# Performance work log

Hardware: AMD Instinct MI355X
Metric: run time of the kernel (lower is better)

Reference implementation:

```python
import jax, jax.numpy as jnp
import numpy as np

NEG_SLOPE = 0.2


def _gat_layer(x, src, dst, W, a_src, a_dst, b, concat):
    """PyG-style GATConv (with self-loops already appended to src/dst).
    x: [N, Fin], W: [Fin, H*D], a_src/a_dst: [H, D], b: [H*D] or [D].
    """
    N = x.shape[0]
    H, D = a_src.shape
    h = (x @ W).reshape(N, H, D)                      # per-head projections
    es = jnp.einsum('nhd,hd->nh', h, a_src)           # alpha_src per node
    ed = jnp.einsum('nhd,hd->nh', h, a_dst)           # alpha_dst per node
    e = jax.nn.leaky_relu(es[src] + ed[dst], NEG_SLOPE)   # [E, H] edge logits
    # segment softmax over incoming edges of each target node
    m = jax.ops.segment_max(e, dst, num_segments=N)       # [N, H]
    ex = jnp.exp(e - m[dst])
    s = jax.ops.segment_sum(ex, dst, num_segments=N)      # [N, H]
    alpha = ex / jnp.where(s > 0, s, 1.0)[dst]            # [E, H]
    out = jax.ops.segment_sum(h[src] * alpha[:, :, None], dst, num_segments=N)  # [N,H,D]
    out = out.reshape(N, H * D) if concat else out.mean(axis=1)
    return out + b


def setup_inputs() -> dict:
    key = jax.random.key(0)
    ks = jax.random.split(key, 16)
    N, E, F_IN, HID, HEADS, NG, NC = 50000, 1000000, 128, 64, 4, 512, 2
    x = jax.random.normal(ks[0], (N, F_IN), dtype=jnp.float32)
    edge_index = jax.random.randint(ks[1], (2, E), 0, N, dtype=jnp.int32)
    batch = jnp.sort(jax.random.randint(ks[2], (N,), 0, NG, dtype=jnp.int32))
    sc = 0.1
    params = {
        'W1': jax.random.normal(ks[3], (F_IN, HEADS * HID), dtype=jnp.float32) * sc,
        'a_src1': jax.random.normal(ks[4], (HEADS, HID), dtype=jnp.float32) * sc,
        'a_dst1': jax.random.normal(ks[5], (HEADS, HID), dtype=jnp.float32) * sc,
        'b1': jnp.zeros((HEADS * HID,), dtype=jnp.float32),
        'W2': jax.random.normal(ks[6], (HEADS * HID, HID), dtype=jnp.float32) * sc,
        'a_src2': jax.random.normal(ks[7], (1, HID), dtype=jnp.float32) * sc,
        'a_dst2': jax.random.normal(ks[8], (1, HID), dtype=jnp.float32) * sc,
        'b2': jnp.zeros((HID,), dtype=jnp.float32),
        'Wc': jax.random.normal(ks[9], (HID, NC), dtype=jnp.float32) * sc,
        'bc': jnp.zeros((NC,), dtype=jnp.float32),
    }
    return {'x': x, 'edge_index': edge_index, 'batch': batch, 'num_graphs': NG, **params}


def reference(x, edge_index, batch, num_graphs, W1, a_src1, a_dst1, b1,
              W2, a_src2, a_dst2, b2, Wc, bc):
    N = x.shape[0]
    # PyG GATConv adds self-loops by default
    loops = jnp.arange(N, dtype=edge_index.dtype)
    src = jnp.concatenate([edge_index[0], loops])
    dst = jnp.concatenate([edge_index[1], loops])
    h = jax.nn.elu(_gat_layer(x, src, dst, W1, a_src1, a_dst1, b1, concat=True))
    h = jax.nn.elu(_gat_layer(h, src, dst, W2, a_src2, a_dst2, b2, concat=False))
    # global mean pool per graph
    sums = jax.ops.segment_sum(h, batch, num_segments=num_graphs)         # [G, HID]
    cnt = jax.ops.segment_sum(jnp.ones((N,), h.dtype), batch, num_segments=num_graphs)
    pooled = sums / jnp.maximum(cnt, 1.0)[:, None]
    return pooled @ Wc + bc
```

## Files before the change

kernel.cpp:

```cpp
#include <hip/hip_runtime.h>

#define NN   50000
#define NE   1000000
#define FIN  128
#define HID  64
#define HEADS 4
#define C1   256
#define NG   512
#define ETOT (NE + NN)
#define BSH  10
#define NBUK 49
#define CHUNK 8192
#define NCHUNK 123

typedef __attribute__((ext_vector_type(8))) short bf16x8;
typedef __attribute__((ext_vector_type(4))) short bf16x4;
typedef __attribute__((ext_vector_type(4))) float f32x4;
typedef __attribute__((ext_vector_type(2))) float f32x2;

__device__ __forceinline__ float lrelu(float v) { return v > 0.f ? v : 0.2f * v; }
__device__ __forceinline__ float eluf(float v)  { return v > 0.f ? v : __expf(v) - 1.f; }

__device__ __forceinline__ unsigned short f2bf(float f) {
    unsigned u = __float_as_uint(f);
    unsigned r = (u + 0x7FFFu + ((u >> 16) & 1u)) >> 16;
    return (unsigned short)r;
}
__device__ __forceinline__ float bf2f(unsigned short b) {
    return __uint_as_float(((unsigned)b) << 16);
}
__device__ __forceinline__ unsigned char f2fp8(float f) {
    int w = __builtin_amdgcn_cvt_pk_fp8_f32(f, f, 0, false);
    return (unsigned char)(w & 0xFF);
}

__global__ __launch_bounds__(256) void k_prep(const float* __restrict__ W1,
                                              const float* __restrict__ W2,
                                              unsigned short* __restrict__ W1t,
                                              unsigned short* __restrict__ W2t) {
    int i = blockIdx.x * 256 + threadIdx.x;
    if (i < FIN * C1) {
        int k = i / C1, c = i % C1;
        W1t[c * FIN + k] = f2bf(W1[i]);
    } else {
        int j = i - FIN * C1;
        if (j < C1 * HID) {
            int k = j / HID, c = j % HID;
            W2t[c * C1 + k] = f2bf(W2[j]);
        }
    }
}

__global__ __launch_bounds__(256) void k_hist(const int* __restrict__ dst,
                                              int* __restrict__ bhist) {
    __shared__ int lh[NBUK];
    int tid = threadIdx.x;
    if (tid < NBUK) lh[tid] = 0;
    __syncthreads();
    for (int e = blockIdx.x * 256 + tid; e < NE; e += gridDim.x * 256)
        atomicAdd(&lh[dst[e] >> BSH], 1);
    __syncthreads();
    if (tid < NBUK) atomicAdd(&bhist[tid], lh[tid]);
}

__global__ void k_bscan(const int* __restrict__ bhist,
                        int* __restrict__ bbase,
                        int* __restrict__ bcur,
                        int* __restrict__ offs) {
    int tid = threadIdx.x;
    int v = (tid < NBUK) ? bhist[tid] : 0;
    int x = v;
    #pragma unroll
    for (int off = 1; off < 64; off <<= 1) {
        int t = __shfl_up(x, off);
        if (tid >= off) x += t;
    }
    if (tid < NBUK) {
        int excl = x - v;
        bbase[tid] = excl;
        bcur[tid] = excl;
    }
    if (tid == NBUK - 1) bbase[NBUK] = x;
    if (tid == 0) offs[NN] = ETOT;
}

__global__ __launch_bounds__(256) void k_part(const int* __restrict__ src,
                                              const int* __restrict__ dst,
                                              int* __restrict__ bcur,
                                              int2* __restrict__ ebuf) {
    __shared__ int lcnt[NBUK];
    __shared__ int gbase[NBUK];
    __shared__ int lrank[NBUK];
    int tid = threadIdx.x;
    int e0 = blockIdx.x * CHUNK;
    int e1 = min(e0 + CHUNK, NE);
    if (tid < NBUK) { lcnt[tid] = 0; lrank[tid] = 0; }
    __syncthreads();
    for (int e = e0 + tid; e < e1; e += 256)
        atomicAdd(&lcnt[dst[e] >> BSH], 1);
    __syncthreads();
    if (tid < NBUK) gbase[tid] = atomicAdd(&bcur[tid], lcnt[tid]);
    __syncthreads();
    for (int e = e0 + tid; e < e1; e += 256) {
        int d = dst[e];
        int b = d >> BSH;
        int r = atomicAdd(&lrank[b], 1);
        ebuf[gbase[b] + r] = make_int2(src[e], d);
    }
}

__global__ __launch_bounds__(1024) void k_bfill(const int2* __restrict__ ebuf,
                                                const int* __restrict__ bbase,
                                                int* __restrict__ offs,
                                                int* __restrict__ colsrc) {
    __shared__ int ldeg[1024];
    __shared__ int lcur[1024];
    __shared__ int ws[16];
    int b = blockIdx.x;
    int tid = threadIdx.x;
    int nbase = b << BSH;
    int ncnt = min(1024, NN - nbase);
    int ebeg = bbase[b], eend = bbase[b + 1];
    ldeg[tid] = 0;
    __syncthreads();
    for (int i = ebeg + tid; i < eend; i += 1024)
        atomicAdd(&ldeg[ebuf[i].y - nbase], 1);
    __syncthreads();
    int v = (tid < ncnt) ? ldeg[tid] + 1 : 0;
    int lane = tid & 63, wv = tid >> 6;
    int x = v;
    #pragma unroll
    for (int off = 1; off < 64; off <<= 1) {
        int t = __shfl_up(x, off);
        if (lane >= off) x += t;
    }
    if (lane == 63) ws[wv] = x;
    __syncthreads();
    if (tid < 16) {
        int y = ws[tid];
        #pragma unroll
        for (int off = 1; off < 16; off <<= 1) {
            int t = __shfl_up(y, off);
            if (tid >= off) y += t;
        }
        ws[tid] = y;
    }
    __syncthreads();
    int base = wv ? ws[wv - 1] : 0;
    int excl = base + x - v;
    int gofs = ebeg + nbase + excl;
    if (tid < ncnt) {
        offs[nbase + tid] = gofs;
        lcur[tid] = gofs;
    }
    __syncthreads();
    for (int i = ebeg + tid; i < eend; i += 1024) {
        int2 ed = ebuf[i];
        int p = atomicAdd(&lcur[ed.y - nbase], 1);
        colsrc[p] = ed.x;
    }
    __syncthreads();
    if (tid < ncnt) colsrc[lcur[tid]] = nbase + tid;
}

__global__ __launch_bounds__(512) void k_gstart(const int* __restrict__ batch,
                                                int* __restrict__ gstart) {
    for (int g = threadIdx.x; g <= NG; g += 512) {
        int lo = 0, hi = NN;
        while (lo < hi) {
            int mid = (lo + hi) >> 1;
            if (batch[mid] < g) lo = mid + 1; else hi = mid;
        }
        gstart[g] = lo;
    }
}

__global__ __launch_bounds__(256) void k_gemm1(const float* __restrict__ x,
                                               const unsigned short* __restrict__ W1t,
                                               const float* __restrict__ asrc,
                                               const float* __restrict__ adst,
                                               unsigned char* __restrict__ h1f,
                                               float* __restrict__ es1,
                                               float* __restrict__ ed1) {
    __shared__ unsigned short Wl[128 * FIN];
    int tid = threadIdx.x;
    int lane = tid & 63, wv = tid >> 6;
    int r0 = (blockIdx.x * 4 + wv) * 16;
    int g = lane >> 4, q = lane & 15;

    int ar = min(r0 + q, NN - 1);
    const float* xr = x + (size_t)ar * FIN;
    bf16x8 afr[4];
    #pragma unroll
    for (int kt = 0; kt < 4; ++kt) {
        float4 u0 = *(const float4*)(xr + kt * 32 + g * 8);
        float4 u1 = *(const float4*)(xr + kt * 32 + g * 8 + 4);
        bf16x8 a;
        a[0] = (short)f2bf(u0.x); a[1] = (short)f2bf(u0.y);
        a[2] = (short)f2bf(u0.z); a[3] = (short)f2bf(u0.w);
        a[4] = (short)f2bf(u1.x); a[5] = (short)f2bf(u1.y);
        a[6] = (short)f2bf(u1.z); a[7] = (short)f2bf(u1.w);
        afr[kt] = a;
    }

    for (int ch = 0; ch < 2; ++ch) {
        if (ch) __syncthreads();
        const uint4* src = (const uint4*)(W1t + (size_t)ch * 128 * FIN);
        #pragma unroll
        for (int i = 0; i < 8; ++i) {
            int idx = tid + i * 256;
            uint4 v = src[idx];
            unsigned byte = (unsigned)idx << 4;
            unsigned dst = byte ^ (((byte >> 8) & 7) << 4);
            *(uint4*)((char*)Wl + dst) = v;
        }
        __syncthreads();

        #pragma unroll
        for (int hh = 0; hh < 2; ++hh) {
            int h = ch * 2 + hh;
            float ps[4] = {0.f, 0.f, 0.f, 0.f};
            float pd[4] = {0.f, 0.f, 0.f, 0.f};
            #pragma unroll
            for (int tl = 0; tl < 4; ++tl) {
                int col = (h * 4 + tl) * 16 + q;
                int cl = col - ch * 128;
                f32x4 acc = {0.f, 0.f, 0.f, 0.f};
                #pragma unroll
                for (int kt = 0; kt < 4; ++kt) {
                    unsigned bb = (unsigned)cl * 256 + kt * 64 + g * 16;
                    bf16x8 b = *(const bf16x8*)((const char*)Wl + (bb ^ (((unsigned)cl & 7) << 4)));
                    acc = __builtin_amdgcn_mfma_f32_16x16x32_bf16(afr[kt], b, acc, 0, 0, 0);
                }
                float av = asrc[col], bv = adst[col];
                #pragma unroll
                for (int j = 0; j < 4; ++j) {
                    int rr = min(r0 + g * 4 + j, NN - 1);
                    h1f[(size_t)rr * C1 + col] = f2fp8(acc[j]);
                    ps[j] += acc[j] * av;
                    pd[j] += acc[j] * bv;
                }
            }
            #pragma unroll
            for (int j = 0; j < 4; ++j) {
                #pragma unroll
                for (int off = 1; off < 16; off <<= 1) {
                    ps[j] += __shfl_xor(ps[j], off);
                    pd[j] += __shfl_xor(pd[j], off);
                }
                if (q == 0) {
                    int rr = min(r0 + g * 4 + j, NN - 1);
                    es1[rr * 4 + h] = ps[j];
                    ed1[rr * 4 + h] = pd[j];
                }
            }
        }
    }
}

__global__ __launch_bounds__(512) void k_agg1(const int* __restrict__ offs,
                                              const int* __restrict__ colsrc,
                                              const unsigned char* __restrict__ h1f,
                                              const float* __restrict__ es1,
                                              const float* __restrict__ ed1,
                                              const float* __restrict__ b1,
                                              unsigned short* __restrict__ h1p) {
    __shared__ int   sls[8][64];
    __shared__ float sla[8][64][4];
    int lane = threadIdx.x & 63, wv = threadIdx.x >> 6;
    int n = blockIdx.x * 8 + wv;
    if (n >= NN) return;
    int beg = offs[n], end = offs[n + 1], deg = end - beg;
    float4 edv = *(const float4*)(ed1 + n * 4);
    int half = lane >> 5, q5 = lane & 31;
    int hd = q5 >> 3;
    f32x2 acc2[4];
    #pragma unroll
    for (int j = 0; j < 4; ++j) acc2[j] = (f32x2){0.f, 0.f};

    if (deg <= 64) {
        int msrc = 0;
        float m0 = 0.f, m1 = 0.f, m2 = 0.f, m3 = 0.f;
        if (lane < deg) {
            msrc = colsrc[beg + lane];
            float4 ev = *(const float4*)(es1 + msrc * 4);
            m0 = __expf(lrelu(ev.x + edv.x));
            m1 = __expf(lrelu(ev.y + edv.y));
            m2 = __expf(lrelu(ev.z + edv.z));
            m3 = __expf(lrelu(ev.w + edv.w));
        }
        float s0 = m0, s1 = m1, s2 = m2, s3 = m3;
        #pragma unroll
        for (int off = 1; off < 64; off <<= 1) {
            s0 += __shfl_xor(s0, off);
            s1 += __shfl_xor(s1, off);
            s2 += __shfl_xor(s2, off);
            s3 += __shfl_xor(s3, off);
        }
        sls[wv][lane] = msrc;
        sla[wv][lane][0] = m0 * (1.f / s0);
        sla[wv][lane][1] = m1 * (1.f / s1);
        sla[wv][lane][2] = m2 * (1.f / s2);
        sla[wv][lane][3] = m3 * (1.f / s3);

        for (int i = 0; i < deg; i += 8) {
            int e0 = (i + half) & 63, e1 = (i + 2 + half) & 63, e2 = (i + 4 + half) & 63, e3 = (i + 6 + half) & 63;
            int   s0i = sls[wv][e0], s1i = sls[wv][e1], s2i = sls[wv][e2], s3i = sls[wv][e3];
            f32x2 a0 = (f32x2){sla[wv][e0][hd], sla[wv][e0][hd]};
            f32x2 a1 = (f32x2){sla[wv][e1][hd], sla[wv][e1][hd]};
            f32x2 a2 = (f32x2){sla[wv][e2][hd], sla[wv][e2][hd]};
            f32x2 a3 = (f32x2){sla[wv][e3][hd], sla[wv][e3][hd]};
            uint2 h0 = *(const uint2*)(h1f + (size_t)s0i * C1 + q5 * 8);
            uint2 h1 = *(const uint2*)(h1f + (size_t)s1i * C1 + q5 * 8);
            uint2 h2 = *(const uint2*)(h1f + (size_t)s2i * C1 + q5 * 8);
            uint2 h3 = *(const uint2*)(h1f + (size_t)s3i * C1 + q5 * 8);
            f32x2 p;
            p = __builtin_amdgcn_cvt_pk_f32_fp8(h0.x, false); acc2[0] += p * a0;
            p = __builtin_amdgcn_cvt_pk_f32_fp8(h0.x, true);  acc2[1] += p * a0;
            p = __builtin_amdgcn_cvt_pk_f32_fp8(h0.y, false); acc2[2] += p * a0;
            p = __builtin_amdgcn_cvt_pk_f32_fp8(h0.y, true);  acc2[3] += p * a0;
            p = __builtin_amdgcn_cvt_pk_f32_fp8(h1.x, false); acc2[0] += p * a1;
            p = __builtin_amdgcn_cvt_pk_f32_fp8(h1.x, true);  acc2[1] += p * a1;
            p = __builtin_amdgcn_cvt_pk_f32_fp8(h1.y, false); acc2[2] += p * a1;
            p = __builtin_amdgcn_cvt_pk_f32_fp8(h1.y, true);  acc2[3] += p * a1;
            p = __builtin_amdgcn_cvt_pk_f32_fp8(h2.x, false); acc2[0] += p * a2;
            p = __builtin_amdgcn_cvt_pk_f32_fp8(h2.x, true);  acc2[1] += p * a2;
            p = __builtin_amdgcn_cvt_pk_f32_fp8(h2.y, false); acc2[2] += p * a2;
            p = __builtin_amdgcn_cvt_pk_f32_fp8(h2.y, true);  acc2[3] += p * a2;
            p = __builtin_amdgcn_cvt_pk_f32_fp8(h3.x, false); acc2[0] += p * a3;
            p = __builtin_amdgcn_cvt_pk_f32_fp8(h3.x, true);  acc2[1] += p * a3;
            p = __builtin_amdgcn_cvt_pk_f32_fp8(h3.y, false); acc2[2] += p * a3;
            p = __builtin_amdgcn_cvt_pk_f32_fp8(h3.y, true);  acc2[3] += p * a3;
        }
    } else {
        float s0 = 0.f, s1 = 0.f, s2 = 0.f, s3 = 0.f;
        for (int i = beg + lane; i < end; i += 64) {
            int s = colsrc[i];
            float4 ev = *(const float4*)(es1 + s * 4);
            s0 += __expf(lrelu(ev.x + edv.x));
            s1 += __expf(lrelu(ev.y + edv.y));
            s2 += __expf(lrelu(ev.z + edv.z));
            s3 += __expf(lrelu(ev.w + edv.w));
        }
        #pragma unroll
        for (int off = 1; off < 64; off <<= 1) {
            s0 += __shfl_xor(s0, off);
            s1 += __shfl_xor(s1, off);
            s2 += __shfl_xor(s2, off);
            s3 += __shfl_xor(s3, off);
        }
        float rr = hd == 0 ? 1.f / s0 : hd == 1 ? 1.f / s1 : hd == 2 ? 1.f / s2 : 1.f / s3;
        float ed_h = hd == 0 ? edv.x : hd == 1 ? edv.y : hd == 2 ? edv.z : edv.w;
        for (int i = beg; i < end; i += 2) {
            int idx = i + half;
            if (idx < end) {
                int s = colsrc[idx];
                float eh = es1[s * 4 + hd] + ed_h;
                float av = __expf(lrelu(eh)) * rr;
                f32x2 a = (f32x2){av, av};
                uint2 hv = *(const uint2*)(h1f + (size_t)s * C1 + q5 * 8);
                f32x2 p;
                p = __builtin_amdgcn_cvt_pk_f32_fp8(hv.x, false); acc2[0] += p * a;
                p = __builtin_amdgcn_cvt_pk_f32_fp8(hv.x, true);  acc2[1] += p * a;
                p = __builtin_amdgcn_cvt_pk_f32_fp8(hv.y, false); acc2[2] += p * a;
                p = __builtin_amdgcn_cvt_pk_f32_fp8(hv.y, true);  acc2[3] += p * a;
            }
        }
    }

    float acc[8];
    #pragma unroll
    for (int j = 0; j < 4; ++j) { acc[2*j] = acc2[j][0]; acc[2*j+1] = acc2[j][1]; }
    #pragma unroll
    for (int j = 0; j < 8; ++j) acc[j] += __shfl_xor(acc[j], 32);

    if (half == 0) {
        float4 bv0 = *(const float4*)(b1 + q5 * 8);
        float4 bv1 = *(const float4*)(b1 + q5 * 8 + 4);
        bf16x8 o;
        o[0] = (short)f2bf(eluf(acc[0] + bv0.x));
        o[1] = (short)f2bf(eluf(acc[1] + bv0.y));
        o[2] = (short)f2bf(eluf(acc[2] + bv0.z));
        o[3] = (short)f2bf(eluf(acc[3] + bv0.w));
        o[4] = (short)f2bf(eluf(acc[4] + bv1.x));
        o[5] = (short)f2bf(eluf(acc[5] + bv1.y));
        o[6] = (short)f2bf(eluf(acc[6] + bv1.z));
        o[7] = (short)f2bf(eluf(acc[7] + bv1.w));
        *(bf16x8*)(h1p + (size_t)n * C1 + q5 * 8) = o;
    }
}

__global__ __launch_bounds__(256) void k_gemm2(const unsigned short* __restrict__ h1p,
                                               const unsigned short* __restrict__ W2t,
                                               const float* __restrict__ as2,
                                               const float* __restrict__ ad2,
                                               unsigned char* __restrict__ h2f,
                                               float* __restrict__ es2,
                                               float* __restrict__ ed2) {
    __shared__ unsigned short Wl[HID * C1];
    int tid = threadIdx.x;
    int lane = tid & 63, wv = tid >> 6;
    int r0 = (blockIdx.x * 4 + wv) * 16;
    int g = lane >> 4, q = lane & 15;

    const uint4* src = (const uint4*)W2t;
    #pragma unroll
    for (int i = 0; i < 8; ++i) {
        int idx = tid + i * 256;
        uint4 v = src[idx];
        unsigned byte = (unsigned)idx << 4;
        unsigned dst = byte ^ (((byte >> 9) & 7) << 4);
        *(uint4*)((char*)Wl + dst) = v;
    }

    int ar = min(r0 + q, NN - 1);
    const unsigned short* arp = h1p + (size_t)ar * C1;
    bf16x8 afr[8];
    #pragma unroll
    for (int kt = 0; kt < 8; ++kt)
        afr[kt] = *(const bf16x8*)(arp + kt * 32 + g * 8);

    __syncthreads();

    float ps[4] = {0.f, 0.f, 0.f, 0.f};
    float pd[4] = {0.f, 0.f, 0.f, 0.f};
    #pragma unroll
    for (int t = 0; t < 4; ++t) {
        int col = t * 16 + q;
        f32x4 acc = {0.f, 0.f, 0.f, 0.f};
        #pragma unroll
        for (int kt = 0; kt < 8; ++kt) {
            unsigned bb = (unsigned)col * 512 + kt * 64 + g * 16;
            bf16x8 b = *(const bf16x8*)((const char*)Wl + (bb ^ (((unsigned)col & 7) << 4)));
            acc = __builtin_amdgcn_mfma_f32_16x16x32_bf16(afr[kt], b, acc, 0, 0, 0);
        }
        float av = as2[col], bv = ad2[col];
        #pragma unroll
        for (int j = 0; j < 4; ++j) {
            int rr = min(r0 + g * 4 + j, NN - 1);
            h2f[(size_t)rr * HID + col] = f2fp8(acc[j]);
            ps[j] += acc[j] * av;
            pd[j] += acc[j] * bv;
        }
    }
    #pragma unroll
    for (int j = 0; j < 4; ++j) {
        #pragma unroll
        for (int off = 1; off < 16; off <<= 1) {
            ps[j] += __shfl_xor(ps[j], off);
            pd[j] += __shfl_xor(pd[j], off);
        }
        if (q == 0) {
            int rr = min(r0 + g * 4 + j, NN - 1);
            es2[rr] = ps[j];
            ed2[rr] = pd[j];
        }
    }
}

__global__ __launch_bounds__(512) void k_agg2(const int* __restrict__ offs,
                                              const int* __restrict__ colsrc,
                                              const unsigned char* __restrict__ h2f,
                                              const float* __restrict__ es2,
                                              const float* __restrict__ ed2,
                                              const float* __restrict__ b2,
                                              float* __restrict__ h3) {
    __shared__ int   sls[8][64];
    __shared__ float sla[8][64];
    int lane = threadIdx.x & 63, wv = threadIdx.x >> 6;
    int n = blockIdx.x * 8 + wv;
    if (n >= NN) return;
    int beg = offs[n], end = offs[n + 1], deg = end - beg;
    float edv = ed2[n];
    int g = lane >> 4, q = lane & 15;
    f32x2 acc2[2];
    acc2[0] = (f32x2){0.f, 0.f};
    acc2[1] = (f32x2){0.f, 0.f};

    if (deg <= 64) {
        int msrc = 0;
        float mex = 0.f;
        if (lane < deg) {
            msrc = colsrc[beg + lane];
            mex = __expf(lrelu(es2[msrc] + edv));
        }
        float ss = mex;
        #pragma unroll
        for (int off = 1; off < 64; off <<= 1) ss += __shfl_xor(ss, off);
        sls[wv][lane] = msrc;
        sla[wv][lane] = mex * (1.f / ss);

        for (int i = 0; i < deg; i += 16) {
            int e0 = (i + g) & 63, e1 = (i + 4 + g) & 63, e2 = (i + 8 + g) & 63, e3 = (i + 12 + g) & 63;
            int   s0i = sls[wv][e0], s1i = sls[wv][e1], s2i = sls[wv][e2], s3i = sls[wv][e3];
            f32x2 a0 = (f32x2){sla[wv][e0], sla[wv][e0]};
            f32x2 a1 = (f32x2){sla[wv][e1], sla[wv][e1]};
            f32x2 a2 = (f32x2){sla[wv][e2], sla[wv][e2]};
            f32x2 a3 = (f32x2){sla[wv][e3], sla[wv][e3]};
            unsigned w0 = *(const unsigned*)(h2f + (size_t)s0i * HID + q * 4);
            unsigned w1 = *(const unsigned*)(h2f + (size_t)s1i * HID + q * 4);
            unsigned w2 = *(const unsigned*)(h2f + (size_t)s2i * HID + q * 4);
            unsigned w3 = *(const unsigned*)(h2f + (size_t)s3i * HID + q * 4);
            f32x2 p;
            p = __builtin_amdgcn_cvt_pk_f32_fp8(w0, false); acc2[0] += p * a0;
            p = __builtin_amdgcn_cvt_pk_f32_fp8(w0, true);  acc2[1] += p * a0;
            p = __builtin_amdgcn_cvt_pk_f32_fp8(w1, false); acc2[0] += p * a1;
            p = __builtin_amdgcn_cvt_pk_f32_fp8(w1, true);  acc2[1] += p * a1;
            p = __builtin_amdgcn_cvt_pk_f32_fp8(w2, false); acc2[0] += p * a2;
            p = __builtin_amdgcn_cvt_pk_f32_fp8(w2, true);  acc2[1] += p * a2;
            p = __builtin_amdgcn_cvt_pk_f32_fp8(w3, false); acc2[0] += p * a3;
            p = __builtin_amdgcn_cvt_pk_f32_fp8(w3, true);  acc2[1] += p * a3;
        }
    } else {
        float ss = 0.f;
        for (int i = beg + lane; i < end; i += 64) {
            int s = colsrc[i];
            ss += __expf(lrelu(es2[s] + edv));
        }
        #pragma unroll
        for (int off = 1; off < 64; off <<= 1) ss += __shfl_xor(ss, off);
        float rs = 1.f / ss;
        for (int i = beg; i < end; i += 4) {
            int idx = i + g;
            if (idx < end) {
                int s = colsrc[idx];
                float av = __expf(lrelu(es2[s] + edv)) * rs;
                f32x2 a = (f32x2){av, av};
                unsigned w = *(const unsigned*)(h2f + (size_t)s * HID + q * 4);
                f32x2 p;
                p = __builtin_amdgcn_cvt_pk_f32_fp8(w, false); acc2[0] += p * a;
                p = __builtin_amdgcn_cvt_pk_f32_fp8(w, true);  acc2[1] += p * a;
            }
        }
    }

    float acc[4] = {acc2[0][0], acc2[0][1], acc2[1][0], acc2[1][1]};
    #pragma unroll
    for (int j = 0; j < 4; ++j) {
        acc[j] += __shfl_xor(acc[j], 16);
        acc[j] += __shfl_xor(acc[j], 32);
    }

    float v0 = __shfl(acc[0], lane >> 2);
    float v1 = __shfl(acc[1], lane >> 2);
    float v2 = __shfl(acc[2], lane >> 2);
    float v3 = __shfl(acc[3], lane >> 2);
    int jj = lane & 3;
    float o = jj == 0 ? v0 : jj == 1 ? v1 : jj == 2 ? v2 : v3;
    h3[(size_t)n * HID + lane] = eluf(o + b2[lane]);
}

__global__ __launch_bounds__(256) void k_poolcls(const float* __restrict__ h3,
                                                 const int* __restrict__ gstart,
                                                 const float* __restrict__ Wc,
                                                 const float* __restrict__ bc,
                                                 float* __restrict__ out) {
    __shared__ float red[4][64];
    int g = blockIdx.x;
    int lane = threadIdx.x & 63, wv = threadIdx.x >> 6;
    int gs = gstart[g], ge = gstart[g + 1];
    float acc = 0.f;
    for (int r = gs + wv; r < ge; r += 4)
        acc += h3[(size_t)r * HID + lane];
    red[wv][lane] = acc;
    __syncthreads();
    if (wv == 0) {
        float p = red[0][lane] + red[1][lane] + red[2][lane] + red[3][lane];
        float c = fmaxf((float)(ge - gs), 1.f);
        p /= c;
        float s0 = p * Wc[lane * 2 + 0];
        float s1 = p * Wc[lane * 2 + 1];
        #pragma unroll
        for (int off = 1; off < 64; off <<= 1) {
            s0 += __shfl_xor(s0, off);
            s1 += __shfl_xor(s1, off);
        }
        if (lane == 0) {
            out[g * 2 + 0] = s0 + bc[0];
            out[g * 2 + 1] = s1 + bc[1];
        }
    }
}

extern "C" void kernel_launch(void* const* d_in, const int* in_sizes, int n_in,
                              void* d_out, int out_size, void* d_ws, size_t ws_size,
                              hipStream_t stream) {
    const float* x   = (const float*)d_in[0];
    const int* ei    = (const int*)d_in[1];
    const int* batch = (const int*)d_in[2];
    const float* W1  = (const float*)d_in[4];
    const float* as1 = (const float*)d_in[5];
    const float* ad1 = (const float*)d_in[6];
    const float* b1  = (const float*)d_in[7];
    const float* W2  = (const float*)d_in[8];
    const float* as2 = (const float*)d_in[9];
    const float* ad2 = (const float*)d_in[10];
    const float* b2  = (const float*)d_in[11];
    const float* Wc  = (const float*)d_in[12];
    const float* bc  = (const float*)d_in[13];
    float* out = (float*)d_out;

    char* p = (char*)d_ws;
    auto alloc = [&](size_t bytes) -> char* {
        char* r = p;
        p += (bytes + 255) & ~(size_t)255;
        return r;
    };
    int* offs    = (int*)alloc((NN + 1) * sizeof(int));
    int* colsrc  = (int*)alloc((size_t)ETOT * sizeof(int));
    int2* ebuf   = (int2*)alloc((size_t)NE * sizeof(int2));
    int* bhist   = (int*)alloc(NBUK * sizeof(int));
    int* bbase   = (int*)alloc((NBUK + 1) * sizeof(int));
    int* bcur    = (int*)alloc(NBUK * sizeof(int));
    int* gstart  = (int*)alloc((NG + 1) * sizeof(int));
    unsigned short* W1t = (unsigned short*)alloc((size_t)FIN * C1 * sizeof(short));
    unsigned short* W2t = (unsigned short*)alloc((size_t)C1 * HID * sizeof(short));
    unsigned char* h1f  = (unsigned char*)alloc((size_t)NN * C1);
    unsigned short* h1p = (unsigned short*)alloc((size_t)NN * C1 * sizeof(short));
    unsigned char* h2f  = (unsigned char*)alloc((size_t)NN * HID);
    float* es1   = (float*)alloc((size_t)NN * 4 * sizeof(float));
    float* ed1   = (float*)alloc((size_t)NN * 4 * sizeof(float));
    float* es2v  = (float*)alloc((size_t)NN * sizeof(float));
    float* ed2v  = (float*)alloc((size_t)NN * sizeof(float));
    float* h3    = (float*)alloc((size_t)NN * HID * sizeof(float));

    hipMemsetAsync(bhist, 0, NBUK * sizeof(int), stream);

    const int* srcA = ei;
    const int* dstA = ei + NE;

    k_prep<<<(FIN * C1 + C1 * HID + 255) / 256, 256, 0, stream>>>(W1, W2, W1t, W2t);
    k_hist<<<256, 256, 0, stream>>>(dstA, bhist);
    k_bscan<<<1, 64, 0, stream>>>(bhist, bbase, bcur, offs);
    k_part<<<NCHUNK, 256, 0, stream>>>(srcA, dstA, bcur, ebuf);
    k_bfill<<<NBUK, 1024, 0, stream>>>(ebuf, bbase, offs, colsrc);
    k_gstart<<<1, 512, 0, stream>>>(batch, gstart);

    k_gemm1<<<(NN / 16 + 3) / 4, 256, 0, stream>>>(x, W1t, as1, ad1, h1f, es1, ed1);
    k_agg1<<<(NN + 7) / 8, 512, 0, stream>>>(offs, colsrc, h1f, es1, ed1, b1, h1p);
    k_gemm2<<<(NN / 16 + 3) / 4, 256, 0, stream>>>(h1p, W2t, as2, ad2, h2f, es2v, ed2v);
    k_agg2<<<(NN + 7) / 8, 512, 0, stream>>>(offs, colsrc, h2f, es2v, ed2v, b2, h3);
    k_poolcls<<<NG, 256, 0, stream>>>(h3, gstart, Wc, bc, out);
}
```

Before: 191.4 us.

## Merge setup kernels into one launch and batch more gathers per aggregation iteration

```diff
diff --git a/kernel.cpp b/kernel.cpp
--- a/kernel.cpp
+++ b/kernel.cpp
@@ -12,6 +12,8 @@
 #define NBUK 49
 #define CHUNK 8192
 #define NCHUNK 123
+#define NPREP 192
+#define NHIST 64
 
 typedef __attribute__((ext_vector_type(8))) short bf16x8;
 typedef __attribute__((ext_vector_type(4))) short bf16x4;
@@ -34,33 +36,46 @@
     return (unsigned char)(w & 0xFF);
 }
 
-__global__ __launch_bounds__(256) void k_prep(const float* __restrict__ W1,
-                                              const float* __restrict__ W2,
-                                              unsigned short* __restrict__ W1t,
-                                              unsigned short* __restrict__ W2t) {
-    int i = blockIdx.x * 256 + threadIdx.x;
-    if (i < FIN * C1) {
-        int k = i / C1, c = i % C1;
-        W1t[c * FIN + k] = f2bf(W1[i]);
+__global__ __launch_bounds__(256) void k_setup(const float* __restrict__ W1,
+                                               const float* __restrict__ W2,
+                                               const int* __restrict__ dst,
+                                               const int* __restrict__ batch,
+                                               unsigned short* __restrict__ W1t,
+                                               unsigned short* __restrict__ W2t,
+                                               int* __restrict__ bhist,
+                                               int* __restrict__ gstart) {
+    int b = blockIdx.x;
+    int tid = threadIdx.x;
+    if (b < NPREP) {
+        int i = b * 256 + tid;
+        if (i < FIN * C1) {
+            int k = i / C1, c = i % C1;
+            W1t[c * FIN + k] = f2bf(W1[i]);
+        } else {
+            int j = i - FIN * C1;
+            if (j < C1 * HID) {
+                int k = j / HID, c = j % HID;
+                W2t[c * C1 + k] = f2bf(W2[j]);
+            }
+        }
+    } else if (b < NPREP + NHIST) {
+        __shared__ int lh[NBUK];
+        if (tid < NBUK) lh[tid] = 0;
+        __syncthreads();
+        for (int e = (b - NPREP) * 256 + tid; e < NE; e += NHIST * 256)
+            atomicAdd(&lh[dst[e] >> BSH], 1);
+        __syncthreads();
+        if (tid < NBUK) atomicAdd(&bhist[tid], lh[tid]);
     } else {
-        int j = i - FIN * C1;
-        if (j < C1 * HID) {
-            int k = j / HID, c = j % HID;
-            W2t[c * C1 + k] = f2bf(W2[j]);
-        }
-    }
-}
-
-__global__ __launch_bounds__(256) void k_hist(const int* __restrict__ dst,
-                                              int* __restrict__ bhist) {
-    __shared__ int lh[NBUK];
-    int tid = threadIdx.x;
-    if (tid < NBUK) lh[tid] = 0;
-    __syncthreads();
-    for (int e = blockIdx.x * 256 + tid; e < NE; e += gridDim.x * 256)
-        atomicAdd(&lh[dst[e] >> BSH], 1);
-    __syncthreads();
-    if (tid < NBUK) atomicAdd(&bhist[tid], lh[tid]);
+        for (int g = tid; g <= NG; g += 256) {
+            int lo = 0, hi = NN;
+            while (lo < hi) {
+                int mid = (lo + hi) >> 1;
+                if (batch[mid] < g) lo = mid + 1; else hi = mid;
+            }
+            gstart[g] = lo;
+        }
+    }
 }
 
 __global__ void k_bscan(const int* __restrict__ bhist,
@@ -161,18 +176,6 @@
     }
     __syncthreads();
     if (tid < ncnt) colsrc[lcur[tid]] = nbase + tid;
-}
-
-__global__ __launch_bounds__(512) void k_gstart(const int* __restrict__ batch,
-                                                int* __restrict__ gstart) {
-    for (int g = threadIdx.x; g <= NG; g += 512) {
-        int lo = 0, hi = NN;
-        while (lo < hi) {
-            int mid = (lo + hi) >> 1;
-            if (batch[mid] < g) lo = mid + 1; else hi = mid;
-        }
-        gstart[g] = lo;
-    }
 }
 
 __global__ __launch_bounds__(256) void k_gemm1(const float* __restrict__ x,
@@ -303,34 +306,25 @@
         sla[wv][lane][2] = m2 * (1.f / s2);
         sla[wv][lane][3] = m3 * (1.f / s3);
 
-        for (int i = 0; i < deg; i += 8) {
-            int e0 = (i + half) & 63, e1 = (i + 2 + half) & 63, e2 = (i + 4 + half) & 63, e3 = (i + 6 + half) & 63;
-            int   s0i = sls[wv][e0], s1i = sls[wv][e1], s2i = sls[wv][e2], s3i = sls[wv][e3];
-            f32x2 a0 = (f32x2){sla[wv][e0][hd], sla[wv][e0][hd]};
-            f32x2 a1 = (f32x2){sla[wv][e1][hd], sla[wv][e1][hd]};
-            f32x2 a2 = (f32x2){sla[wv][e2][hd], sla[wv][e2][hd]};
-            f32x2 a3 = (f32x2){sla[wv][e3][hd], sla[wv][e3][hd]};
-            uint2 h0 = *(const uint2*)(h1f + (size_t)s0i * C1 + q5 * 8);
-            uint2 h1 = *(const uint2*)(h1f + (size_t)s1i * C1 + q5 * 8);
-            uint2 h2 = *(const uint2*)(h1f + (size_t)s2i * C1 + q5 * 8);
-            uint2 h3 = *(const uint2*)(h1f + (size_t)s3i * C1 + q5 * 8);
-            f32x2 p;
-            p = __builtin_amdgcn_cvt_pk_f32_fp8(h0.x, false); acc2[0] += p * a0;
-            p = __builtin_amdgcn_cvt_pk_f32_fp8(h0.x, true);  acc2[1] += p * a0;
-            p = __builtin_amdgcn_cvt_pk_f32_fp8(h0.y, false); acc2[2] += p * a0;
-            p = __builtin_amdgcn_cvt_pk_f32_fp8(h0.y, true);  acc2[3] += p * a0;
-            p = __builtin_amdgcn_cvt_pk_f32_fp8(h1.x, false); acc2[0] += p * a1;
-            p = __builtin_amdgcn_cvt_pk_f32_fp8(h1.x, true);  acc2[1] += p * a1;
-            p = __builtin_amdgcn_cvt_pk_f32_fp8(h1.y, false); acc2[2] += p * a1;
-            p = __builtin_amdgcn_cvt_pk_f32_fp8(h1.y, true);  acc2[3] += p * a1;
-            p = __builtin_amdgcn_cvt_pk_f32_fp8(h2.x, false); acc2[0] += p * a2;
-            p = __builtin_amdgcn_cvt_pk_f32_fp8(h2.x, true);  acc2[1] += p * a2;
-            p = __builtin_amdgcn_cvt_pk_f32_fp8(h2.y, false); acc2[2] += p * a2;
-            p = __builtin_amdgcn_cvt_pk_f32_fp8(h2.y, true);  acc2[3] += p * a2;
-            p = __builtin_amdgcn_cvt_pk_f32_fp8(h3.x, false); acc2[0] += p * a3;
-            p = __builtin_amdgcn_cvt_pk_f32_fp8(h3.x, true);  acc2[1] += p * a3;
-            p = __builtin_amdgcn_cvt_pk_f32_fp8(h3.y, false); acc2[2] += p * a3;
-            p = __builtin_amdgcn_cvt_pk_f32_fp8(h3.y, true);  acc2[3] += p * a3;
+        for (int i = 0; i < deg; i += 16) {
+            uint2 hv[8];
+            float a[8];
+            #pragma unroll
+            for (int u = 0; u < 8; ++u) {
+                int ee = (i + 2 * u + half) & 63;
+                int s = sls[wv][ee];
+                a[u] = sla[wv][ee][hd];
+                hv[u] = *(const uint2*)(h1f + (size_t)s * C1 + q5 * 8);
+            }
+            #pragma unroll
+            for (int u = 0; u < 8; ++u) {
+                f32x2 av = (f32x2){a[u], a[u]};
+                f32x2 p;
+                p = __builtin_amdgcn_cvt_pk_f32_fp8(hv[u].x, false); acc2[0] += p * av;
+                p = __builtin_amdgcn_cvt_pk_f32_fp8(hv[u].x, true);  acc2[1] += p * av;
+                p = __builtin_amdgcn_cvt_pk_f32_fp8(hv[u].y, false); acc2[2] += p * av;
+                p = __builtin_amdgcn_cvt_pk_f32_fp8(hv[u].y, true);  acc2[3] += p * av;
+            }
         }
     } else {
         float s0 = 0.f, s1 = 0.f, s2 = 0.f, s3 = 0.f;
@@ -490,26 +484,23 @@
         sls[wv][lane] = msrc;
         sla[wv][lane] = mex * (1.f / ss);
 
-        for (int i = 0; i < deg; i += 16) {
-            int e0 = (i + g) & 63, e1 = (i + 4 + g) & 63, e2 = (i + 8 + g) & 63, e3 = (i + 12 + g) & 63;
-            int   s0i = sls[wv][e0], s1i = sls[wv][e1], s2i = sls[wv][e2], s3i = sls[wv][e3];
-            f32x2 a0 = (f32x2){sla[wv][e0], sla[wv][e0]};
-            f32x2 a1 = (f32x2){sla[wv][e1], sla[wv][e1]};
-            f32x2 a2 = (f32x2){sla[wv][e2], sla[wv][e2]};
-            f32x2 a3 = (f32x2){sla[wv][e3], sla[wv][e3]};
-            unsigned w0 = *(const unsigned*)(h2f + (size_t)s0i * HID + q * 4);
-            unsigned w1 = *(const unsigned*)(h2f + (size_t)s1i * HID + q * 4);
-            unsigned w2 = *(const unsigned*)(h2f + (size_t)s2i * HID + q * 4);
-            unsigned w3 = *(const unsigned*)(h2f + (size_t)s3i * HID + q * 4);
-            f32x2 p;
-            p = __builtin_amdgcn_cvt_pk_f32_fp8(w0, false); acc2[0] += p * a0;
-            p = __builtin_amdgcn_cvt_pk_f32_fp8(w0, true);  acc2[1] += p * a0;
-            p = __builtin_amdgcn_cvt_pk_f32_fp8(w1, false); acc2[0] += p * a1;
-            p = __builtin_amdgcn_cvt_pk_f32_fp8(w1, true);  acc2[1] += p * a1;
-            p = __builtin_amdgcn_cvt_pk_f32_fp8(w2, false); acc2[0] += p * a2;
-            p = __builtin_amdgcn_cvt_pk_f32_fp8(w2, true);  acc2[1] += p * a2;
-            p = __builtin_amdgcn_cvt_pk_f32_fp8(w3, false); acc2[0] += p * a3;
-            p = __builtin_amdgcn_cvt_pk_f32_fp8(w3, true);  acc2[1] += p * a3;
+        for (int i = 0; i < deg; i += 32) {
+            unsigned w[8];
+            float a[8];
+            #pragma unroll
+            for (int u = 0; u < 8; ++u) {
+                int ee = (i + 4 * u + g) & 63;
+                int s = sls[wv][ee];
+                a[u] = sla[wv][ee];
+                w[u] = *(const unsigned*)(h2f + (size_t)s * HID + q * 4);
+            }
+            #pragma unroll
+            for (int u = 0; u < 8; ++u) {
+                f32x2 av = (f32x2){a[u], a[u]};
+                f32x2 p;
+                p = __builtin_amdgcn_cvt_pk_f32_fp8(w[u], false); acc2[0] += p * av;
+                p = __builtin_amdgcn_cvt_pk_f32_fp8(w[u], true);  acc2[1] += p * av;
+            }
         }
     } else {
         float ss = 0.f;
@@ -629,12 +620,10 @@
     const int* srcA = ei;
     const int* dstA = ei + NE;
 
-    k_prep<<<(FIN * C1 + C1 * HID + 255) / 256, 256, 0, stream>>>(W1, W2, W1t, W2t);
-    k_hist<<<256, 256, 0, stream>>>(dstA, bhist);
+    k_setup<<<NPREP + NHIST + 1, 256, 0, stream>>>(W1, W2, dstA, batch, W1t, W2t, bhist, gstart);
     k_bscan<<<1, 64, 0, stream>>>(bhist, bbase, bcur, offs);
     k_part<<<NCHUNK, 256, 0, stream>>>(srcA, dstA, bcur, ebuf);
     k_bfill<<<NBUK, 1024, 0, stream>>>(ebuf, bbase, offs, colsrc);
-    k_gstart<<<1, 512, 0, stream>>>(batch, gstart);
 
     k_gemm1<<<(NN / 16 + 3) / 4, 256, 0, stream>>>(x, W1t, as1, ad1, h1f, es1, ed1);
     k_agg1<<<(NN + 7) / 8, 512, 0, stream>>>(offs, colsrc, h1f, es1, ed1, b1, h1p);
```

New measurement: 193.8 us. No clear change (+1.3%).

## Merge setup kernels, co-schedule partition with GEMM1, pack edges, store h3 as bf16

Applied to the files above, without the earlier changes.

```diff
diff --git a/kernel.cpp b/kernel.cpp
--- a/kernel.cpp
+++ b/kernel.cpp
@@ -12,6 +12,9 @@
 #define NBUK 49
 #define CHUNK 8192
 #define NCHUNK 123
+#define NPREP 192
+#define NHIST 64
+#define NGEMM1 782
 
 typedef __attribute__((ext_vector_type(8))) short bf16x8;
 typedef __attribute__((ext_vector_type(4))) short bf16x4;
@@ -34,33 +37,46 @@
     return (unsigned char)(w & 0xFF);
 }
 
-__global__ __launch_bounds__(256) void k_prep(const float* __restrict__ W1,
-                                              const float* __restrict__ W2,
-                                              unsigned short* __restrict__ W1t,
-                                              unsigned short* __restrict__ W2t) {
-    int i = blockIdx.x * 256 + threadIdx.x;
-    if (i < FIN * C1) {
-        int k = i / C1, c = i % C1;
-        W1t[c * FIN + k] = f2bf(W1[i]);
+__global__ __launch_bounds__(256) void k_setup(const float* __restrict__ W1,
+                                               const float* __restrict__ W2,
+                                               const int* __restrict__ dst,
+                                               const int* __restrict__ batch,
+                                               unsigned short* __restrict__ W1t,
+                                               unsigned short* __restrict__ W2t,
+                                               int* __restrict__ bhist,
+                                               int* __restrict__ gstart) {
+    int b = blockIdx.x;
+    int tid = threadIdx.x;
+    if (b < NPREP) {
+        int i = b * 256 + tid;
+        if (i < FIN * C1) {
+            int k = i / C1, c = i % C1;
+            W1t[c * FIN + k] = f2bf(W1[i]);
+        } else {
+            int j = i - FIN * C1;
+            if (j < C1 * HID) {
+                int k = j / HID, c = j % HID;
+                W2t[c * C1 + k] = f2bf(W2[j]);
+            }
+        }
+    } else if (b < NPREP + NHIST) {
+        __shared__ int lh[NBUK];
+        if (tid < NBUK) lh[tid] = 0;
+        __syncthreads();
+        for (int e = (b - NPREP) * 256 + tid; e < NE; e += NHIST * 256)
+            atomicAdd(&lh[dst[e] >> BSH], 1);
+        __syncthreads();
+        if (tid < NBUK) atomicAdd(&bhist[tid], lh[tid]);
     } else {
-        int j = i - FIN * C1;
-        if (j < C1 * HID) {
-            int k = j / HID, c = j % HID;
-            W2t[c * C1 + k] = f2bf(W2[j]);
-        }
-    }
-}
-
-__global__ __launch_bounds__(256) void k_hist(const int* __restrict__ dst,
-                                              int* __restrict__ bhist) {
-    __shared__ int lh[NBUK];
-    int tid = threadIdx.x;
-    if (tid < NBUK) lh[tid] = 0;
-    __syncthreads();
-    for (int e = blockIdx.x * 256 + tid; e < NE; e += gridDim.x * 256)
-        atomicAdd(&lh[dst[e] >> BSH], 1);
-    __syncthreads();
-    if (tid < NBUK) atomicAdd(&bhist[tid], lh[tid]);
+        for (int g = tid; g <= NG; g += 256) {
+            int lo = 0, hi = NN;
+            while (lo < hi) {
+                int mid = (lo + hi) >> 1;
+                if (batch[mid] < g) lo = mid + 1; else hi = mid;
+            }
+            gstart[g] = lo;
+        }
+    }
 }
 
 __global__ void k_bscan(const int* __restrict__ bhist,
@@ -84,108 +100,45 @@
     if (tid == 0) offs[NN] = ETOT;
 }
 
-__global__ __launch_bounds__(256) void k_part(const int* __restrict__ src,
-                                              const int* __restrict__ dst,
-                                              int* __restrict__ bcur,
-                                              int2* __restrict__ ebuf) {
-    __shared__ int lcnt[NBUK];
-    __shared__ int gbase[NBUK];
-    __shared__ int lrank[NBUK];
+__global__ __launch_bounds__(256) void k_part_gemm1(const int* __restrict__ srcA,
+                                                    const int* __restrict__ dstA,
+                                                    int* __restrict__ bcur,
+                                                    int* __restrict__ ebuf,
+                                                    const float* __restrict__ x,
+                                                    const unsigned short* __restrict__ W1t,
+                                                    const float* __restrict__ asrc,
+                                                    const float* __restrict__ adst,
+                                                    unsigned char* __restrict__ h1f,
+                                                    float* __restrict__ es1,
+                                                    float* __restrict__ ed1) {
+    __shared__ int lsh[128 * FIN / 2];
     int tid = threadIdx.x;
-    int e0 = blockIdx.x * CHUNK;
-    int e1 = min(e0 + CHUNK, NE);
-    if (tid < NBUK) { lcnt[tid] = 0; lrank[tid] = 0; }
-    __syncthreads();
-    for (int e = e0 + tid; e < e1; e += 256)
-        atomicAdd(&lcnt[dst[e] >> BSH], 1);
-    __syncthreads();
-    if (tid < NBUK) gbase[tid] = atomicAdd(&bcur[tid], lcnt[tid]);
-    __syncthreads();
-    for (int e = e0 + tid; e < e1; e += 256) {
-        int d = dst[e];
-        int b = d >> BSH;
-        int r = atomicAdd(&lrank[b], 1);
-        ebuf[gbase[b] + r] = make_int2(src[e], d);
-    }
-}
-
-__global__ __launch_bounds__(1024) void k_bfill(const int2* __restrict__ ebuf,
-                                                const int* __restrict__ bbase,
-                                                int* __restrict__ offs,
-                                                int* __restrict__ colsrc) {
-    __shared__ int ldeg[1024];
-    __shared__ int lcur[1024];
-    __shared__ int ws[16];
-    int b = blockIdx.x;
-    int tid = threadIdx.x;
-    int nbase = b << BSH;
-    int ncnt = min(1024, NN - nbase);
-    int ebeg = bbase[b], eend = bbase[b + 1];
-    ldeg[tid] = 0;
-    __syncthreads();
-    for (int i = ebeg + tid; i < eend; i += 1024)
-        atomicAdd(&ldeg[ebuf[i].y - nbase], 1);
-    __syncthreads();
-    int v = (tid < ncnt) ? ldeg[tid] + 1 : 0;
+
+    if (blockIdx.x < NCHUNK) {
+        int* lcnt  = lsh;
+        int* gbase = lsh + NBUK;
+        int* lrank = lsh + 2 * NBUK;
+        int e0 = blockIdx.x * CHUNK;
+        int e1 = min(e0 + CHUNK, NE);
+        if (tid < NBUK) { lcnt[tid] = 0; lrank[tid] = 0; }
+        __syncthreads();
+        for (int e = e0 + tid; e < e1; e += 256)
+            atomicAdd(&lcnt[dstA[e] >> BSH], 1);
+        __syncthreads();
+        if (tid < NBUK) gbase[tid] = atomicAdd(&bcur[tid], lcnt[tid]);
+        __syncthreads();
+        for (int e = e0 + tid; e < e1; e += 256) {
+            int d = dstA[e];
+            int b = d >> BSH;
+            int r = atomicAdd(&lrank[b], 1);
+            ebuf[gbase[b] + r] = ((d & 1023) << 17) | srcA[e];
+        }
+        return;
+    }
+
+    unsigned short* Wl = (unsigned short*)lsh;
     int lane = tid & 63, wv = tid >> 6;
-    int x = v;
-    #pragma unroll
-    for (int off = 1; off < 64; off <<= 1) {
-        int t = __shfl_up(x, off);
-        if (lane >= off) x += t;
-    }
-    if (lane == 63) ws[wv] = x;
-    __syncthreads();
-    if (tid < 16) {
-        int y = ws[tid];
-        #pragma unroll
-        for (int off = 1; off < 16; off <<= 1) {
-            int t = __shfl_up(y, off);
-            if (tid >= off) y += t;
-        }
-        ws[tid] = y;
-    }
-    __syncthreads();
-    int base = wv ? ws[wv - 1] : 0;
-    int excl = base + x - v;
-    int gofs = ebeg + nbase + excl;
-    if (tid < ncnt) {
-        offs[nbase + tid] = gofs;
-        lcur[tid] = gofs;
-    }
-    __syncthreads();
-    for (int i = ebeg + tid; i < eend; i += 1024) {
-        int2 ed = ebuf[i];
-        int p = atomicAdd(&lcur[ed.y - nbase], 1);
-        colsrc[p] = ed.x;
-    }
-    __syncthreads();
-    if (tid < ncnt) colsrc[lcur[tid]] = nbase + tid;
-}
-
-__global__ __launch_bounds__(512) void k_gstart(const int* __restrict__ batch,
-                                                int* __restrict__ gstart) {
-    for (int g = threadIdx.x; g <= NG; g += 512) {
-        int lo = 0, hi = NN;
-        while (lo < hi) {
-            int mid = (lo + hi) >> 1;
-            if (batch[mid] < g) lo = mid + 1; else hi = mid;
-        }
-        gstart[g] = lo;
-    }
-}
-
-__global__ __launch_bounds__(256) void k_gemm1(const float* __restrict__ x,
-                                               const unsigned short* __restrict__ W1t,
-                                               const float* __restrict__ asrc,
-                                               const float* __restrict__ adst,
-                                               unsigned char* __restrict__ h1f,
-                                               float* __restrict__ es1,
-                                               float* __restrict__ ed1) {
-    __shared__ unsigned short Wl[128 * FIN];
-    int tid = threadIdx.x;
-    int lane = tid & 63, wv = tid >> 6;
-    int r0 = (blockIdx.x * 4 + wv) * 16;
+    int r0 = ((blockIdx.x - NCHUNK) * 4 + wv) * 16;
     int g = lane >> 4, q = lane & 15;
 
     int ar = min(r0 + q, NN - 1);
@@ -258,6 +211,60 @@
     }
 }
 
+__global__ __launch_bounds__(1024) void k_bfill(const int* __restrict__ ebuf,
+                                                const int* __restrict__ bbase,
+                                                int* __restrict__ offs,
+                                                int* __restrict__ colsrc) {
+    __shared__ int ldeg[1024];
+    __shared__ int lcur[1024];
+    __shared__ int ws[16];
+    int b = blockIdx.x;
+    int tid = threadIdx.x;
+    int nbase = b << BSH;
+    int ncnt = min(1024, NN - nbase);
+    int ebeg = bbase[b], eend = bbase[b + 1];
+    ldeg[tid] = 0;
+    __syncthreads();
+    for (int i = ebeg + tid; i < eend; i += 1024)
+        atomicAdd(&ldeg[ebuf[i] >> 17], 1);
+    __syncthreads();
+    int v = (tid < ncnt) ? ldeg[tid] + 1 : 0;
+    int lane = tid & 63, wv = tid >> 6;
+    int x = v;
+    #pragma unroll
+    for (int off = 1; off < 64; off <<= 1) {
+        int t = __shfl_up(x, off);
+        if (lane >= off) x += t;
+    }
+    if (lane == 63) ws[wv] = x;
+    __syncthreads();
+    if (tid < 16) {
+        int y = ws[tid];
+        #pragma unroll
+        for (int off = 1; off < 16; off <<= 1) {
+            int t = __shfl_up(y, off);
+            if (tid >= off) y += t;
+        }
+        ws[tid] = y;
+    }
+    __syncthreads();
+    int base = wv ? ws[wv - 1] : 0;
+    int excl = base + x - v;
+    int gofs = ebeg + nbase + excl;
+    if (tid < ncnt) {
+        offs[nbase + tid] = gofs;
+        lcur[tid] = gofs;
+    }
+    __syncthreads();
+    for (int i = ebeg + tid; i < eend; i += 1024) {
+        int pe = ebuf[i];
+        int p = atomicAdd(&lcur[pe >> 17], 1);
+        colsrc[p] = pe & 0x1FFFF;
+    }
+    __syncthreads();
+    if (tid < ncnt) colsrc[lcur[tid]] = nbase + tid;
+}
+
 __global__ __launch_bounds__(512) void k_agg1(const int* __restrict__ offs,
                                               const int* __restrict__ colsrc,
                                               const unsigned char* __restrict__ h1f,
@@ -464,7 +471,7 @@
                                               const float* __restrict__ es2,
                                               const float* __restrict__ ed2,
                                               const float* __restrict__ b2,
-                                              float* __restrict__ h3) {
+                                              unsigned short* __restrict__ h3) {
     __shared__ int   sls[8][64];
     __shared__ float sla[8][64];
     int lane = threadIdx.x & 63, wv = threadIdx.x >> 6;
@@ -547,10 +554,10 @@
     float v3 = __shfl(acc[3], lane >> 2);
     int jj = lane & 3;
     float o = jj == 0 ? v0 : jj == 1 ? v1 : jj == 2 ? v2 : v3;
-    h3[(size_t)n * HID + lane] = eluf(o + b2[lane]);
-}
-
-__global__ __launch_bounds__(256) void k_poolcls(const float* __restrict__ h3,
+    h3[(size_t)n * HID + lane] = f2bf(eluf(o + b2[lane]));
+}
+
+__global__ __launch_bounds__(256) void k_poolcls(const unsigned short* __restrict__ h3,
                                                  const int* __restrict__ gstart,
                                                  const float* __restrict__ Wc,
                                                  const float* __restrict__ bc,
@@ -561,7 +568,7 @@
     int gs = gstart[g], ge = gstart[g + 1];
     float acc = 0.f;
     for (int r = gs + wv; r < ge; r += 4)
-        acc += h3[(size_t)r * HID + lane];
+        acc += bf2f(h3[(size_t)r * HID + lane]);
     red[wv][lane] = acc;
     __syncthreads();
     if (wv == 0) {
@@ -608,7 +615,7 @@
     };
     int* offs    = (int*)alloc((NN + 1) * sizeof(int));
     int* colsrc  = (int*)alloc((size_t)ETOT * sizeof(int));
-    int2* ebuf   = (int2*)alloc((size_t)NE * sizeof(int2));
+    int* ebuf    = (int*)alloc((size_t)NE * sizeof(int));
     int* bhist   = (int*)alloc(NBUK * sizeof(int));
     int* bbase   = (int*)alloc((NBUK + 1) * sizeof(int));
     int* bcur    = (int*)alloc(NBUK * sizeof(int));
@@ -622,21 +629,19 @@
     float* ed1   = (float*)alloc((size_t)NN * 4 * sizeof(float));
     float* es2v  = (float*)alloc((size_t)NN * sizeof(float));
     float* ed2v  = (float*)alloc((size_t)NN * sizeof(float));
-    float* h3    = (float*)alloc((size_t)NN * HID * sizeof(float));
+    unsigned short* h3 = (unsigned short*)alloc((size_t)NN * HID * sizeof(short));
 
     hipMemsetAsync(bhist, 0, NBUK * sizeof(int), stream);
 
     const int* srcA = ei;
     const int* dstA = ei + NE;
 
-    k_prep<<<(FIN * C1 + C1 * HID + 255) / 256, 256, 0, stream>>>(W1, W2, W1t, W2t);
-    k_hist<<<256, 256, 0, stream>>>(dstA, bhist);
+    k_setup<<<NPREP + NHIST + 1, 256, 0, stream>>>(W1, W2, dstA, batch, W1t, W2t, bhist, gstart);
     k_bscan<<<1, 64, 0, stream>>>(bhist, bbase, bcur, offs);
-    k_part<<<NCHUNK, 256, 0, stream>>>(srcA, dstA, bcur, ebuf);
+    k_part_gemm1<<<NCHUNK + NGEMM1, 256, 0, stream>>>(srcA, dstA, bcur, ebuf,
+                                                      x, W1t, as1, ad1, h1f, es1, ed1);
     k_bfill<<<NBUK, 1024, 0, stream>>>(ebuf, bbase, offs, colsrc);
-    k_gstart<<<1, 512, 0, stream>>>(batch, gstart);
-
-    k_gemm1<<<(NN / 16 + 3) / 4, 256, 0, stream>>>(x, W1t, as1, ad1, h1f, es1, ed1);
+
     k_agg1<<<(NN + 7) / 8, 512, 0, stream>>>(offs, colsrc, h1f, es1, ed1, b1, h1p);
     k_gemm2<<<(NN / 16 + 3) / 4, 256, 0, stream>>>(h1p, W2t, as2, ad2, h2f, es2v, ed2v);
     k_agg2<<<(NN + 7) / 8, 512, 0, stream>>>(offs, colsrc, h2f, es2v, ed2v, b2, h3);
```

Result: faster. 172.4 us (-9.9%).
